# Optimization experiments

Measured on AMD Instinct MI355X. Metric: run time of the kernel, lower is better.

## Reference

```python
import jax, jax.numpy as jnp
import numpy as np

V, E, H, L, T, B, K = 50000, 256, 512, 2, 256, 64, 32


def setup_inputs() -> dict:
    key = jax.random.key(0)
    ks = iter(jax.random.split(key, 64))
    def p(shape, scale=0.05):
        return jax.random.normal(next(ks), shape, jnp.float32) * scale
    inp = {"sentences": jax.random.randint(next(ks), (T, B), 0, V)}
    inp["emb"] = p((V, E), 0.1)
    in_sizes = [E, 2 * H]
    for l in range(L):
        for d in ("f", "r"):
            inp[f"w_ih_l{l}{d}"] = p((4 * H, in_sizes[l]))
            inp[f"w_hh_l{l}{d}"] = p((4 * H, H))
            inp[f"b_ih_l{l}{d}"] = p((4 * H,))
            inp[f"b_hh_l{l}{d}"] = p((4 * H,))
    inp["W_out"] = p((K, 2 * H))
    inp["b_out"] = p((K,))
    inp["transitions"] = p((K, K), 0.1)
    inp["start_trans"] = p((K,), 0.1)
    inp["stop_trans"] = p((K,), 0.1)
    return inp


def _lstm_dir(x, w_ih, w_hh, b_ih, b_hh, reverse):
    # x: (T, B, D). PyTorch gate order: i, f, g, o.
    Hd = w_hh.shape[1]
    xp = jnp.einsum('tbd,gd->tbg', x, w_ih) + b_ih + b_hh  # precompute input proj
    def step(carry, xt):
        h, c = carry
        g = xt + h @ w_hh.T
        i, f, gg, o = jnp.split(g, 4, axis=-1)
        c = jax.nn.sigmoid(f) * c + jax.nn.sigmoid(i) * jnp.tanh(gg)
        h = jax.nn.sigmoid(o) * jnp.tanh(c)
        return (h, c), h
    z = jnp.zeros((x.shape[1], Hd), x.dtype)
    _, hs = jax.lax.scan(step, (z, z), xp, reverse=reverse)
    return hs


def _forward(sentences, emb, layer_params, W_out, b_out, transitions, start_trans, stop_trans):
    x = emb[sentences]  # (T, B, E); dropout is identity at inference
    for (pf, pr) in layer_params:
        hf = _lstm_dir(x, *pf, reverse=False)
        hr = _lstm_dir(x, *pr, reverse=True)
        x = jnp.concatenate([hf, hr], axis=-1)  # (T, B, 2H)
    feats = jnp.einsum('tbh,kh->tbk', x, W_out) + b_out  # (T, B, K)

    # Viterbi: R[b, j, k] = transitions[j, k] + dp[b, k] + feat[b, j]
    dp0 = start_trans + feats[0]
    def vstep(dp, feat):
        R = transitions[None] + dp[:, None, :] + feat[:, :, None]
        return R.max(-1), R.argmax(-1)
    dp, bps = jax.lax.scan(vstep, dp0, feats[1:])  # bps: (T-1, B, K)
    dp = dp + stop_trans
    scores = dp.max(-1)
    last = dp.argmax(-1)
    def back(tag, bp_t):
        prev = jnp.take_along_axis(bp_t, tag[:, None], axis=1)[:, 0]
        return prev, prev
    _, pre = jax.lax.scan(back, last, bps, reverse=True)  # (T-1, B), in time order
    paths = jnp.concatenate([pre, last[None]], axis=0)  # (T, B)
    return scores, paths


def reference(sentences, emb,
              w_ih_l0f, w_hh_l0f, b_ih_l0f, b_hh_l0f,
              w_ih_l0r, w_hh_l0r, b_ih_l0r, b_hh_l0r,
              w_ih_l1f, w_hh_l1f, b_ih_l1f, b_hh_l1f,
              w_ih_l1r, w_hh_l1r, b_ih_l1r, b_hh_l1r,
              W_out, b_out, transitions, start_trans, stop_trans):
    layer_params = [
        ((w_ih_l0f, w_hh_l0f, b_ih_l0f, b_hh_l0f), (w_ih_l0r, w_hh_l0r, b_ih_l0r, b_hh_l0r)),
        ((w_ih_l1f, w_hh_l1f, b_ih_l1f, b_hh_l1f), (w_ih_l1r, w_hh_l1r, b_ih_l1r, b_hh_l1r)),
    ]
    return _forward(sentences, emb, layer_params, W_out, b_out, transitions, start_trans, stop_trans)
```

## Files before the change

kernel.cpp:

```cpp
#include <hip/hip_runtime.h>
#include <cstdint>
#include <cstddef>

#define T_ 256
#define B_ 64
#define E_ 256
#define H_ 512
#define NTAG 32
#define CHK 32
#define HSLOT 33

static constexpr size_t OX1  = 0;
static constexpr size_t SX1  = (size_t)T_*256*B_*4;
static constexpr size_t OX2  = OX1 + SX1;
static constexpr size_t SX2  = SX1;
static constexpr size_t OX0  = OX2;
static constexpr size_t OXP  = OX2 + SX2;
static constexpr size_t SXPC = (size_t)CHK*2048*B_;
static constexpr size_t SXP  = 2*SXPC;
static constexpr size_t OWHH0 = OXP + SXP;
static constexpr size_t SWHH  = (size_t)2*512*512*4;
static constexpr size_t OWHH1 = OWHH0 + SWHH;
static constexpr size_t OWIH0 = OWHH1 + SWHH;
static constexpr size_t SWIH0 = (size_t)2*2048*256;
static constexpr size_t OWIH1 = OWIH0 + SWIH0;
static constexpr size_t SWIH1 = (size_t)2*2048*1024;
static constexpr size_t OWOUT = OWIH1 + SWIH1;
static constexpr size_t SWOUT = (size_t)1024*32;
static constexpr size_t OHH   = OWOUT + SWOUT;
static constexpr size_t SHHL  = (size_t)2*HSLOT*32768;
static constexpr size_t SHH   = 2*SHHL;
static constexpr size_t OCB   = OHH + SHH;
static constexpr size_t SCB   = (size_t)2*2*512*64;
static constexpr size_t OBAR  = OCB + SCB;
static constexpr size_t SBAR  = (size_t)2*2*128*16;
static constexpr size_t OFE   = OBAR + SBAR;
static constexpr size_t SFE   = (size_t)T_*B_*NTAG;
static constexpr size_t OBP   = OFE + SFE;
static constexpr size_t SBP   = (size_t)T_*B_*NTAG/4;
static constexpr size_t WS_FLOATS = OBP + SBP;

__device__ __forceinline__ float sigf(float x){ return 1.0f/(1.0f + expf(-x)); }

__global__ void pack_whh(const float* __restrict__ w, float* __restrict__ out){
  int id = blockIdx.x*256 + threadIdx.x;
  int gate = id & 3, k = (id>>2) & 511, u = id >> 11;
  out[id] = w[((size_t)gate*512 + u)*512 + k];
}
__global__ void pack_wih(const float* __restrict__ w, float* __restrict__ out, int K, int kshift){
  int id = blockIdx.x*256 + threadIdx.x;
  int k = id & (K-1); int jj = (id>>kshift)&15; int g = id>>(kshift+4);
  out[((size_t)g*K + k)*16 + jj] = w[(size_t)(g*16+jj)*K + k];
}
__global__ void pack_wout(const float* __restrict__ w, float* __restrict__ out){
  int id = blockIdx.x*256 + threadIdx.x;
  int k = id & 1023, jj = id>>10;
  out[k*32 + jj] = w[id];
}

__global__ void gather_emb(const int* __restrict__ sent, const float* __restrict__ emb,
                           float* __restrict__ x0){
  int t = blockIdx.x; int lane = threadIdx.x & 63; int w = threadIdx.x >> 6;
  int s = sent[t*B_ + lane];
  const float4* er = (const float4*)emb + (size_t)s*(E_/4);
  float4* xo = (float4*)x0 + (size_t)t*64*64;
  #pragma unroll
  for (int q=0; q<16; ++q){
    int e4 = w*16 + q;
    xo[e4*64 + lane] = er[e4];
  }
}

__global__ __launch_bounds__(256) void proj_kernel(
    const float* __restrict__ xin, const float* __restrict__ wpack,
    const float* __restrict__ bihf, const float* __restrict__ bhhf,
    const float* __restrict__ bihr, const float* __restrict__ bhhr,
    float* __restrict__ xp, int K, int t0){
  int i = blockIdx.x, jg = blockIdx.y, dir = blockIdx.z;
  int t = dir ? (T_-1 - (t0 + i)) : (t0 + i);
  int lane = threadIdx.x & 63;
  int w = __builtin_amdgcn_readfirstlane((int)threadIdx.x) >> 6;
  int kq = K >> 2;
  int n4 = kq >> 2;
  int k40 = (w*kq) >> 2;
  const float4* xi = (const float4*)xin + (size_t)t*(K>>2)*64;
  size_t pstride = (size_t)K*16;
  const float* wp = wpack + (size_t)dir*2048*K + (size_t)(jg*2)*pstride + (size_t)w*kq*16;
  float acc[2][16];
  #pragma unroll
  for (int p=0;p<2;p++)
    #pragma unroll
    for (int jj=0;jj<16;jj++) acc[p][jj] = 0.f;
  for (int k4=0; k4<n4; ++k4){
    float4 h = xi[(k40+k4)*64 + lane];
    float hv[4] = {h.x, h.y, h.z, h.w};
    #pragma unroll
    for (int p=0;p<2;p++){
      const float* wv = wp + p*pstride + k4*64;
      #pragma unroll
      for (int ii=0;ii<4;ii++)
        #pragma unroll
        for (int jj=0;jj<16;jj++)
          acc[p][jj] = fmaf(wv[ii*16+jj], hv[ii], acc[p][jj]);
    }
  }
  __shared__ float red[4][32][64];
  #pragma unroll
  for (int p=0;p<2;p++)
    #pragma unroll
    for (int jj=0;jj<16;jj++) red[w][p*16+jj][lane] = acc[p][jj];
  __syncthreads();
  const float* b1 = dir ? bihr : bihf;
  const float* b2 = dir ? bhhr : bhhf;
  float* xpd = xp + (size_t)dir*SXPC + (size_t)i*2048*64;
  #pragma unroll
  for (int q=0;q<8;q++){
    int rr = w*8 + q;
    float v = red[0][rr][lane] + red[1][rr][lane] + red[2][rr][lane] + red[3][rr][lane];
    int row = jg*32 + rr;
    v += b1[row] + b2[row];
    xpd[(size_t)row*64 + lane] = v;
  }
}

__global__ __launch_bounds__(256) void rec_kernel(
    const float* __restrict__ xp, const float* __restrict__ whh,
    float* __restrict__ xout, float* __restrict__ hh, float* __restrict__ cb0,
    int* __restrict__ flags, int step0, int nsteps){
  int bid = blockIdx.x;
  int dir = bid & 1, g = bid >> 1;
  int lane = threadIdx.x & 63;
  int w = __builtin_amdgcn_readfirstlane((int)threadIdx.x >> 6);
  int u = g*4 + w;
  const float* xpd = xp + (size_t)dir*SXPC;
  const float4* wv4 = (const float4*)(whh + (size_t)dir*1048576 + (size_t)u*2048);
  float* hhd = hh + (size_t)dir*((size_t)HSLOT*32768);
  float* cb = cb0 + dir*32768;
  int* fl = flags + dir*(128*16);
  __shared__ float hlds[256];
  float c = cb[u*64 + lane];
  size_t xb = ((size_t)u)*64 + lane;
  float x0v = xpd[xb], x1v = xpd[xb+512*64], x2v = xpd[xb+1024*64], x3v = xpd[xb+1536*64];
  for (int s=0; s<nsteps; ++s){
    int gstep = step0 + s;
    int t = dir ? (T_-1-gstep) : gstep;
    const float4* hp = (const float4*)(hhd + (size_t)(gstep % HSLOT)*32768);
    float a0=0.f, a1=0.f, a2=0.f, a3=0.f;
    #pragma unroll 8
    for (int k4=0;k4<128;k4++){
      float4 h4 = hp[k4*64 + lane];
      float4 wa = wv4[k4*4+0], wb = wv4[k4*4+1], wc = wv4[k4*4+2], wd = wv4[k4*4+3];
      a0 = fmaf(wa.x, h4.x, a0); a1 = fmaf(wa.y, h4.x, a1);
      a2 = fmaf(wa.z, h4.x, a2); a3 = fmaf(wa.w, h4.x, a3);
      a0 = fmaf(wb.x, h4.y, a0); a1 = fmaf(wb.y, h4.y, a1);
      a2 = fmaf(wb.z, h4.y, a2); a3 = fmaf(wb.w, h4.y, a3);
      a0 = fmaf(wc.x, h4.z, a0); a1 = fmaf(wc.y, h4.z, a1);
      a2 = fmaf(wc.z, h4.z, a2); a3 = fmaf(wc.w, h4.z, a3);
      a0 = fmaf(wd.x, h4.w, a0); a1 = fmaf(wd.y, h4.w, a1);
      a2 = fmaf(wd.z, h4.w, a2); a3 = fmaf(wd.w, h4.w, a3);
    }
    float g0 = a0 + x0v, g1 = a1 + x1v, g2 = a2 + x2v, g3 = a3 + x3v;
    float iv = sigf(g0), fv = sigf(g1);
    float gg = tanhf(g2), ov = sigf(g3);
    c = fv*c + iv*gg;
    float h = ov*tanhf(c);
    hlds[lane*4 + w] = h;
    __syncthreads();
    if (w == 0){
      float4 hv4 = ((const float4*)hlds)[lane];
      union { float4 f; unsigned long long q[2]; } uu; uu.f = hv4;
      unsigned long long* dst = (unsigned long long*)
          (hhd + (size_t)((gstep+1) % HSLOT)*32768 + (size_t)g*256 + (size_t)lane*4);
      __hip_atomic_store(dst+0, uu.q[0], __ATOMIC_RELAXED, __HIP_MEMORY_SCOPE_AGENT);
      __hip_atomic_store(dst+1, uu.q[1], __ATOMIC_RELAXED, __HIP_MEMORY_SCOPE_AGENT);
    } else if (w == 1){
      float4 hv4 = ((const float4*)hlds)[lane];
      float4* xo = (float4*)(xout + (size_t)t*65536 + (size_t)(dir*128 + g)*256);
      xo[lane] = hv4;
    }
    if (s < nsteps-1){
      if (w == 0){
        asm volatile("s_waitcnt vmcnt(0)" ::: "memory");
      }
      __syncthreads();
      if (threadIdx.x == 0)
        __hip_atomic_store(&fl[g*16], gstep+1, __ATOMIC_RELAXED, __HIP_MEMORY_SCOPE_AGENT);
      size_t xb2 = ((size_t)(s+1)*2048 + u)*64 + lane;
      x0v = xpd[xb2]; x1v = xpd[xb2+512*64]; x2v = xpd[xb2+1024*64]; x3v = xpd[xb2+1536*64];
      int tid = threadIdx.x;
      if (tid < 128){
        int target = gstep+1;
        int spins = 0;
        while (__hip_atomic_load(&fl[tid*16], __ATOMIC_RELAXED, __HIP_MEMORY_SCOPE_AGENT) < target){
          __builtin_amdgcn_s_sleep(1);
          if (++spins > (1<<22)) break;
        }
      }
      __syncthreads();
      asm volatile("" ::: "memory");
    }
  }
  cb[u*64 + lane] = c;
}

__global__ __launch_bounds__(256) void feats_kernel(
    const float* __restrict__ x2, const float* __restrict__ wout,
    const float* __restrict__ bout, float* __restrict__ feats){
  int t = blockIdx.x; int lane = threadIdx.x & 63;
  int w = __builtin_amdgcn_readfirstlane((int)threadIdx.x) >> 6;
  const float4* xi = (const float4*)x2 + (size_t)t*16384;
  const float* wp = wout + (size_t)w*256*32;
  float acc[32];
  #pragma unroll
  for (int j=0;j<32;j++) acc[j] = 0.f;
  for (int k4=0;k4<64;k4++){
    float4 h = xi[(w*64 + k4)*64 + lane];
    float hv[4] = {h.x, h.y, h.z, h.w};
    const float* wv = wp + k4*128;
    #pragma unroll
    for (int ii=0;ii<4;ii++)
      #pragma unroll
      for (int j=0;j<32;j++)
        acc[j] = fmaf(wv[ii*32+j], hv[ii], acc[j]);
  }
  __shared__ float red[4][32][64];
  #pragma unroll
  for (int j=0;j<32;j++) red[w][j][lane] = acc[j];
  __syncthreads();
  __shared__ float tr[64*33];
  #pragma unroll
  for (int q=0;q<8;q++){
    int j = w*8 + q;
    float v = red[0][j][lane]+red[1][j][lane]+red[2][j][lane]+red[3][j][lane] + bout[j];
    tr[lane*33 + j] = v;
  }
  __syncthreads();
  float* fo = feats + (size_t)t*2048;
  int tid = threadIdx.x;
  #pragma unroll
  for (int q=0;q<8;q++){
    int idx = tid*8 + q;
    fo[idx] = tr[(idx>>5)*33 + (idx&31)];
  }
}

__global__ __launch_bounds__(64) void viterbi_kernel(
    const float* __restrict__ feats, const float* __restrict__ trans,
    const float* __restrict__ start, const float* __restrict__ stop,
    unsigned char* __restrict__ bp, float* __restrict__ out){
  int lane = threadIdx.x & 63;
  int b = blockIdx.x*2 + (lane>>5);
  int j = lane & 31;
  int base = lane & 32;
  float tr[32];
  #pragma unroll
  for (int k=0;k<32;k++) tr[k] = trans[j*32+k];
  float dp = start[j] + feats[b*32 + j];
  for (int t=1;t<T_;t++){
    float best = __shfl(dp, base, 64) + tr[0];
    int arg = 0;
    #pragma unroll
    for (int k=1;k<32;k++){
      float v = __shfl(dp, base + k, 64) + tr[k];
      if (v > best){ best = v; arg = k; }
    }
    dp = best + feats[((size_t)t*64 + b)*32 + j];
    bp[(size_t)(t-1)*2048 + b*32 + j] = (unsigned char)arg;
  }
  dp += stop[j];
  float bv = dp; int bi = j;
  #pragma unroll
  for (int off=1; off<32; off<<=1){
    float ov = __shfl_xor(bv, off, 64);
    int oi   = __shfl_xor(bi, off, 64);
    if (ov > bv || (ov == bv && oi < bi)){ bv = ov; bi = oi; }
  }
  if (j == 0){
    out[b] = bv;
    int cur = bi;
    out[64 + 255*64 + b] = (float)cur;
    for (int t=254;t>=0;t--){
      cur = bp[(size_t)t*2048 + b*32 + cur];
      out[64 + t*64 + b] = (float)cur;
    }
  }
}

extern "C" void kernel_launch(void* const* d_in, const int* in_sizes, int n_in,
                              void* d_out, int out_size, void* d_ws, size_t ws_size,
                              hipStream_t stream){
  const int*   sent      = (const int*)  d_in[0];
  const float* emb       = (const float*)d_in[1];
  const float* w_ih_l0f  = (const float*)d_in[2];
  const float* w_hh_l0f  = (const float*)d_in[3];
  const float* b_ih_l0f  = (const float*)d_in[4];
  const float* b_hh_l0f  = (const float*)d_in[5];
  const float* w_ih_l0r  = (const float*)d_in[6];
  const float* w_hh_l0r  = (const float*)d_in[7];
  const float* b_ih_l0r  = (const float*)d_in[8];
  const float* b_hh_l0r  = (const float*)d_in[9];
  const float* w_ih_l1f  = (const float*)d_in[10];
  const float* w_hh_l1f  = (const float*)d_in[11];
  const float* b_ih_l1f  = (const float*)d_in[12];
  const float* b_hh_l1f  = (const float*)d_in[13];
  const float* w_ih_l1r  = (const float*)d_in[14];
  const float* w_hh_l1r  = (const float*)d_in[15];
  const float* b_ih_l1r  = (const float*)d_in[16];
  const float* b_hh_l1r  = (const float*)d_in[17];
  const float* W_out     = (const float*)d_in[18];
  const float* b_out     = (const float*)d_in[19];
  const float* trans     = (const float*)d_in[20];
  const float* start_t   = (const float*)d_in[21];
  const float* stop_t    = (const float*)d_in[22];
  float* ws  = (float*)d_ws;
  float* out = (float*)d_out;

  if (ws_size < WS_FLOATS * sizeof(float)) return;

  hipMemsetAsync(ws + OHH, 0, (SHH + SCB + SBAR)*sizeof(float), stream);

  pack_whh<<<4096,256,0,stream>>>(w_hh_l0f, ws + OWHH0);
  pack_whh<<<4096,256,0,stream>>>(w_hh_l0r, ws + OWHH0 + 1048576);
  pack_whh<<<4096,256,0,stream>>>(w_hh_l1f, ws + OWHH1);
  pack_whh<<<4096,256,0,stream>>>(w_hh_l1r, ws + OWHH1 + 1048576);
  pack_wih<<<2048,256,0,stream>>>(w_ih_l0f, ws + OWIH0,           256, 8);
  pack_wih<<<2048,256,0,stream>>>(w_ih_l0r, ws + OWIH0 + 524288,  256, 8);
  pack_wih<<<8192,256,0,stream>>>(w_ih_l1f, ws + OWIH1,           1024, 10);
  pack_wih<<<8192,256,0,stream>>>(w_ih_l1r, ws + OWIH1 + 2097152, 1024, 10);
  pack_wout<<<128,256,0,stream>>>(W_out, ws + OWOUT);

  gather_emb<<<256,256,0,stream>>>(sent, emb, ws + OX0);

  const int NCH = T_ / CHK;
  dim3 gp(CHK, 64, 2);
  int* bar = (int*)(ws + OBAR);

  for (int c = 0; c < NCH; ++c){
    proj_kernel<<<gp,256,0,stream>>>(ws+OX0, ws+OWIH0,
                                     b_ih_l0f,b_hh_l0f,b_ih_l0r,b_hh_l0r,
                                     ws+OXP, 256, c*CHK);
    rec_kernel<<<256,256,0,stream>>>(ws+OXP, ws+OWHH0, ws+OX1,
                                     ws+OHH, ws+OCB, bar, c*CHK, CHK);
  }
  for (int c = 0; c < NCH; ++c){
    proj_kernel<<<gp,256,0,stream>>>(ws+OX1, ws+OWIH1,
                                     b_ih_l1f,b_hh_l1f,b_ih_l1r,b_hh_l1r,
                                     ws+OXP, 1024, c*CHK);
    rec_kernel<<<256,256,0,stream>>>(ws+OXP, ws+OWHH1, ws+OX2,
                                     ws+OHH+SHHL, ws+OCB+65536,
                                     bar + 4096, c*CHK, CHK);
  }
  feats_kernel<<<256,256,0,stream>>>(ws+OX2, ws+OWOUT, b_out, ws+OFE);
  viterbi_kernel<<<32,64,0,stream>>>(ws+OFE, trans, start_t, stop_t,
                                     (unsigned char*)(ws+OBP), out);
}
```

Baseline: 9.113 ms.

## Split recurrent matvec over K across waves with LDS reduction

The recurrent kernel now gives each wave a quarter of the hidden dimension and has it compute partial dot products for all four hidden units of the block. The partial sums are reduced through shared memory before the gate nonlinearities. Each wave previously read the whole h vector, and now each reads only its slice of h into registers, which cuts redundant global h loads per step. The cost is an extra LDS reduction and barrier, plus higher register pressure from 32 float4 h registers, handled by launch_bounds(256,1). The projection grid axes are also swapped so that consecutive blocks walk gate groups within one timestep.

```diff
diff --git a/kernel.cpp b/kernel.cpp
--- a/kernel.cpp
+++ b/kernel.cpp
@@ -76,7 +76,7 @@
     const float* __restrict__ bihf, const float* __restrict__ bhhf,
     const float* __restrict__ bihr, const float* __restrict__ bhhr,
     float* __restrict__ xp, int K, int t0){
-  int i = blockIdx.x, jg = blockIdx.y, dir = blockIdx.z;
+  int jg = blockIdx.x, i = blockIdx.y, dir = blockIdx.z;
   int t = dir ? (T_-1 - (t0 + i)) : (t0 + i);
   int lane = threadIdx.x & 63;
   int w = __builtin_amdgcn_readfirstlane((int)threadIdx.x) >> 6;
@@ -123,7 +123,7 @@
   }
 }
 
-__global__ __launch_bounds__(256) void rec_kernel(
+__global__ __launch_bounds__(256,1) void rec_kernel(
     const float* __restrict__ xp, const float* __restrict__ whh,
     float* __restrict__ xout, float* __restrict__ hh, float* __restrict__ cb0,
     int* __restrict__ flags, int step0, int nsteps){
@@ -131,37 +131,58 @@
   int dir = bid & 1, g = bid >> 1;
   int lane = threadIdx.x & 63;
   int w = __builtin_amdgcn_readfirstlane((int)threadIdx.x >> 6);
-  int u = g*4 + w;
   const float* xpd = xp + (size_t)dir*SXPC;
-  const float4* wv4 = (const float4*)(whh + (size_t)dir*1048576 + (size_t)u*2048);
+  const float* wbase = whh + (size_t)dir*1048576 + (size_t)g*4*2048;
   float* hhd = hh + (size_t)dir*((size_t)HSLOT*32768);
   float* cb = cb0 + dir*32768;
   int* fl = flags + dir*(128*16);
+  __shared__ float red[4][16][64];
   __shared__ float hlds[256];
-  float c = cb[u*64 + lane];
-  size_t xb = ((size_t)u)*64 + lane;
-  float x0v = xpd[xb], x1v = xpd[xb+512*64], x2v = xpd[xb+1024*64], x3v = xpd[xb+1536*64];
+  int uo = g*4 + w;
+  float c = cb[uo*64 + lane];
+  size_t xb = ((size_t)uo)*64 + lane;
+  float x0v = xpd[xb], x1v = xpd[xb+32768], x2v = xpd[xb+65536], x3v = xpd[xb+98304];
   for (int s=0; s<nsteps; ++s){
     int gstep = step0 + s;
     int t = dir ? (T_-1-gstep) : gstep;
     const float4* hp = (const float4*)(hhd + (size_t)(gstep % HSLOT)*32768);
-    float a0=0.f, a1=0.f, a2=0.f, a3=0.f;
-    #pragma unroll 8
-    for (int k4=0;k4<128;k4++){
-      float4 h4 = hp[k4*64 + lane];
-      float4 wa = wv4[k4*4+0], wb = wv4[k4*4+1], wc = wv4[k4*4+2], wd = wv4[k4*4+3];
-      a0 = fmaf(wa.x, h4.x, a0); a1 = fmaf(wa.y, h4.x, a1);
-      a2 = fmaf(wa.z, h4.x, a2); a3 = fmaf(wa.w, h4.x, a3);
-      a0 = fmaf(wb.x, h4.y, a0); a1 = fmaf(wb.y, h4.y, a1);
-      a2 = fmaf(wb.z, h4.y, a2); a3 = fmaf(wb.w, h4.y, a3);
-      a0 = fmaf(wc.x, h4.z, a0); a1 = fmaf(wc.y, h4.z, a1);
-      a2 = fmaf(wc.z, h4.z, a2); a3 = fmaf(wc.w, h4.z, a3);
-      a0 = fmaf(wd.x, h4.w, a0); a1 = fmaf(wd.y, h4.w, a1);
-      a2 = fmaf(wd.z, h4.w, a2); a3 = fmaf(wd.w, h4.w, a3);
-    }
-    float g0 = a0 + x0v, g1 = a1 + x1v, g2 = a2 + x2v, g3 = a3 + x3v;
-    float iv = sigf(g0), fv = sigf(g1);
-    float gg = tanhf(g2), ov = sigf(g3);
+    float4 hreg[32];
+    #pragma unroll
+    for (int i=0;i<32;i++) hreg[i] = hp[(w*32+i)*64 + lane];
+    float acc[4][4];
+    #pragma unroll
+    for (int cu=0;cu<4;cu++)
+      #pragma unroll
+      for (int gt=0;gt<4;gt++) acc[cu][gt]=0.f;
+    #pragma unroll
+    for (int i=0;i<32;i++){
+      float hv[4] = {hreg[i].x, hreg[i].y, hreg[i].z, hreg[i].w};
+      #pragma unroll
+      for (int cu=0; cu<4; cu++){
+        const float4* wr = (const float4*)(wbase + (size_t)cu*2048 + (size_t)(w*128 + i*4)*4);
+        #pragma unroll
+        for (int kk=0;kk<4;kk++){
+          float4 w4 = wr[kk];
+          acc[cu][0] = fmaf(w4.x, hv[kk], acc[cu][0]);
+          acc[cu][1] = fmaf(w4.y, hv[kk], acc[cu][1]);
+          acc[cu][2] = fmaf(w4.z, hv[kk], acc[cu][2]);
+          acc[cu][3] = fmaf(w4.w, hv[kk], acc[cu][3]);
+        }
+      }
+    }
+    #pragma unroll
+    for (int cu=0;cu<4;cu++)
+      #pragma unroll
+      for (int gt=0;gt<4;gt++) red[w][cu*4+gt][lane] = acc[cu][gt];
+    __syncthreads();
+    float gv[4];
+    #pragma unroll
+    for (int gt=0;gt<4;gt++)
+      gv[gt] = red[0][w*4+gt][lane] + red[1][w*4+gt][lane]
+             + red[2][w*4+gt][lane] + red[3][w*4+gt][lane];
+    gv[0] += x0v; gv[1] += x1v; gv[2] += x2v; gv[3] += x3v;
+    float iv = sigf(gv[0]), fv = sigf(gv[1]);
+    float gg = tanhf(gv[2]), ov = sigf(gv[3]);
     c = fv*c + iv*gg;
     float h = ov*tanhf(c);
     hlds[lane*4 + w] = h;
@@ -185,8 +206,8 @@
       __syncthreads();
       if (threadIdx.x == 0)
         __hip_atomic_store(&fl[g*16], gstep+1, __ATOMIC_RELAXED, __HIP_MEMORY_SCOPE_AGENT);
-      size_t xb2 = ((size_t)(s+1)*2048 + u)*64 + lane;
-      x0v = xpd[xb2]; x1v = xpd[xb2+512*64]; x2v = xpd[xb2+1024*64]; x3v = xpd[xb2+1536*64];
+      size_t xb2 = ((size_t)(s+1)*2048 + uo)*64 + lane;
+      x0v = xpd[xb2]; x1v = xpd[xb2+32768]; x2v = xpd[xb2+65536]; x3v = xpd[xb2+98304];
       int tid = threadIdx.x;
       if (tid < 128){
         int target = gstep+1;
@@ -200,7 +221,7 @@
       asm volatile("" ::: "memory");
     }
   }
-  cb[u*64 + lane] = c;
+  cb[uo*64 + lane] = c;
 }
 
 __global__ __launch_bounds__(256) void feats_kernel(
@@ -332,7 +353,7 @@
   gather_emb<<<256,256,0,stream>>>(sent, emb, ws + OX0);
 
   const int NCH = T_ / CHK;
-  dim3 gp(CHK, 64, 2);
+  dim3 gp(64, CHK, 2);
   int* bar = (int*)(ws + OBAR);
 
   for (int c = 0; c < NCH; ++c){
```

Result: no change. 8.940 ms (-1.9%).
